# Performance work log

Measured on AMD Instinct MI355X. Metric: run time of the kernel, lower is better.

## Reference

```python
import jax, jax.numpy as jnp
import numpy as np

NUM_EXPERTS = 64
Z_LOSS_COEF = 0.001
AUX_LOSS_COEF = 0.001
GROUPS, TOKENS = 64, 8192


def setup_inputs() -> dict:
    key = jax.random.key(0)
    k1, = jax.random.split(key, 1)
    router_logits = jax.random.normal(k1, (GROUPS, TOKENS, NUM_EXPERTS), dtype=jnp.float32)
    attention_mask = jnp.ones((GROUPS, TOKENS), dtype=jnp.int32)  # unused by forward, kept for fidelity
    return {"router_logits": router_logits, "attention_mask": attention_mask, "expert_capacity": 160}


def reference(router_logits, attention_mask, expert_capacity):
    g, t, e = router_logits.shape

    # --- router z-loss: mean over (groups, tokens) of logsumexp^2 ---
    log_z = jax.nn.logsumexp(router_logits, axis=-1)            # [g, t]
    z_loss = jnp.sum(log_z * log_z) / (g * t)

    # --- softmax probs ---
    router_probs = jax.nn.softmax(router_logits, axis=-1)       # [g, t, e]

    # --- recompute expert indices with capacity masking ---
    expert_index = jnp.argmax(router_probs, axis=-1)            # [g, t]
    oh = jax.nn.one_hot(expert_index, e, dtype=jnp.int32)       # [g, t, e]
    token_priority = jnp.cumsum(oh, axis=-2)                    # running count per expert
    capacity_mask = token_priority <= expert_capacity
    oh_masked = oh * capacity_mask.astype(jnp.int32)
    # if token dropped (row all zero), argmax -> 0, matching torch semantics
    expert_index = jnp.argmax(oh_masked, axis=-1)               # [g, t]

    # --- load-balancing aux loss ---
    expert_mask = jax.nn.one_hot(expert_index, e, dtype=jnp.float32)  # [g, t, e]
    tokens_per_group_and_expert = jnp.mean(expert_mask, axis=-2)       # [g, e]
    router_prob_per_group_and_expert = jnp.mean(router_probs, axis=-2) # [g, e]
    aux_loss = jnp.mean(tokens_per_group_and_expert * router_prob_per_group_and_expert) * (e ** 2)

    return Z_LOSS_COEF * z_loss + AUX_LOSS_COEF * aux_loss
```

## Files before the change

### kernel.cpp

```cpp
#include <hip/hip_runtime.h>

#define NG 64
#define NT 8192
#define NE 64
#define Z_COEF 0.001f
#define A_COEF 0.001f

#define BLK 512
#define ITERS 4
#define TPW 64
#define TPB 512
#define NBLK (NG * (NT / TPB))

#define LOG2E 1.44269504088896340736f
#define LN2   0.69314718055994530942f
#define BIGIDX 1048576

#define DPP_XOR1  0xB1
#define DPP_XOR2  0x4E
#define DPP_HMIRR 0x141
#define DPP_MIRR  0x140

template <int CTRL>
__device__ __forceinline__ float fdpp(float x) {
    return __int_as_float(__builtin_amdgcn_mov_dpp(__float_as_int(x), CTRL, 0xF, 0xF, true));
}
template <int CTRL>
__device__ __forceinline__ int idpp(int x) {
    return __builtin_amdgcn_mov_dpp(x, CTRL, 0xF, 0xF, true);
}


__global__ __launch_bounds__(BLK) void router_main(
    const float* __restrict__ logits,
    float* __restrict__ pps,
    unsigned int* __restrict__ pcnt,
    float* __restrict__ pz)
{
    const int tid  = threadIdx.x;
    const int lane = tid & 63;
    const int wv   = tid >> 6;
    const int c    = lane & 15;
    const int cb   = c << 2;

    const int g     = blockIdx.x >> 4;
    const int tbase = (blockIdx.x & 15) * TPB + wv * TPW;

    const float* p0 = logits + ((size_t)g * NT + tbase) * NE + lane * 4;

    __shared__ float        s_ps[NE];
    __shared__ unsigned int s_cnt[NE];
    __shared__ float        s_z;
    if (tid < NE) { s_ps[tid] = 0.f; s_cnt[tid] = 0u; }
    if (tid == 0) s_z = 0.f;
    __syncthreads();

    float accp[4] = {0.f, 0.f, 0.f, 0.f};
    float accz = 0.f;

    for (int it = 0; it < ITERS; ++it) {
        const float* pi = p0 + (size_t)it * 1024;
        float4 cur[4];
#pragma unroll
        for (int k = 0; k < 4; ++k)
            cur[k] = *reinterpret_cast<const float4*>(pi + k * 256);

#pragma unroll
        for (int k = 0; k < 4; ++k) {
            const float v0 = cur[k].x, v1 = cur[k].y, v2 = cur[k].z, v3 = cur[k].w;

            float m = fmaxf(fmaxf(v0, v1), fmaxf(v2, v3));
            m = fmaxf(m, fdpp<DPP_XOR1>(m));
            m = fmaxf(m, fdpp<DPP_XOR2>(m));
            m = fmaxf(m, fdpp<DPP_HMIRR>(m));
            m = fmaxf(m, fdpp<DPP_MIRR>(m));

            const float e0 = exp2f((v0 - m) * LOG2E);
            const float e1 = exp2f((v1 - m) * LOG2E);
            const float e2 = exp2f((v2 - m) * LOG2E);
            const float e3 = exp2f((v3 - m) * LOG2E);
            float s = (e0 + e1) + (e2 + e3);

            int me = BIGIDX;
            if (v3 == m) me = cb + 3;
            if (v2 == m) me = cb + 2;
            if (v1 == m) me = cb + 1;
            if (v0 == m) me = cb + 0;
            me = min(me, idpp<DPP_XOR1>(me));
            me = min(me, idpp<DPP_XOR2>(me));
            me = min(me, idpp<DPP_HMIRR>(me));
            me = min(me, idpp<DPP_MIRR>(me));

            s += fdpp<DPP_XOR1>(s);
            s += fdpp<DPP_XOR2>(s);
            s += fdpp<DPP_HMIRR>(s);
            s += fdpp<DPP_MIRR>(s);

            const float inv = __builtin_amdgcn_rcpf(s);
            accp[0] = fmaf(e0, inv, accp[0]);
            accp[1] = fmaf(e1, inv, accp[1]);
            accp[2] = fmaf(e2, inv, accp[2]);
            accp[3] = fmaf(e3, inv, accp[3]);

            const float lz = fmaf(__log2f(s), LN2, m);
            accz = fmaf(lz, lz, accz);

            if (c == 0)
                atomicAdd(&s_cnt[me], 1u);
        }
    }

#pragma unroll
    for (int j = 0; j < 4; ++j) {
        accp[j] += __shfl_xor(accp[j], 16);
        accp[j] += __shfl_xor(accp[j], 32);
    }
    if (lane < 16) {
#pragma unroll
        for (int j = 0; j < 4; ++j) atomicAdd(&s_ps[(c << 2) + j], accp[j]);
    }
    accz += __shfl_xor(accz, 1);
    accz += __shfl_xor(accz, 2);
    accz += __shfl_xor(accz, 4);
    accz += __shfl_xor(accz, 8);
    accz += __shfl_xor(accz, 16);
    accz += __shfl_xor(accz, 32);
    if (lane == 0) atomicAdd(&s_z, accz * 0.0625f);
    __syncthreads();

    const int row = blockIdx.x;
    if (tid < NE) {
        pps [row * NE + tid] = s_ps[tid];
        pcnt[row * NE + tid] = s_cnt[tid];
    }
    if (tid == 0) pz[row] = s_z;
}

__global__ __launch_bounds__(1024) void router_final(
    const float* __restrict__ pps,
    const unsigned int* __restrict__ pcnt,
    const float* __restrict__ pz,
    const int* __restrict__ capp,
    float* __restrict__ out)
{
    const int tid  = threadIdx.x;
    const int lane = tid & 63;
    const int w    = tid >> 6;
    const unsigned int C = (unsigned int)(*capp);

    __shared__ float s_aux[16];
    __shared__ float s_zz[16];

    float acc = 0.f;
#pragma unroll
    for (int gi = 0; gi < NG / 16; ++gi) {
        const int g = w + gi * 16;
        unsigned int n = 0u;
        float        P = 0.f;
#pragma unroll
        for (int b = 0; b < 16; ++b) {
            const int row = g * 16 + b;
            n += pcnt[row * NE + lane];
            P += pps [row * NE + lane];
        }
        float ovf = (n > C) ? (float)(n - C) : 0.f;
#pragma unroll
        for (int off = 1; off <= 32; off <<= 1) ovf += __shfl_xor(ovf, off);
        float ce = fminf((float)n, (float)C);
        if (lane == 0) ce += ovf;
        acc += ce * P;
    }
#pragma unroll
    for (int off = 1; off <= 32; off <<= 1) acc += __shfl_xor(acc, off);
    if (lane == 0) s_aux[w] = acc;

    float zz = pz[tid];
#pragma unroll
    for (int off = 1; off <= 32; off <<= 1) zz += __shfl_xor(zz, off);
    if (lane == 0) s_zz[w] = zz;
    __syncthreads();

    if (tid == 0) {
        float A = 0.f, Z = 0.f;
#pragma unroll
        for (int i = 0; i < 16; ++i) { A += s_aux[i]; Z += s_zz[i]; }
        const float aux_loss = A * ((float)NE / ((float)NG * (float)NT * (float)NT));
        const float z_loss   = Z / ((float)NG * (float)NT);
        out[0] = Z_COEF * z_loss + A_COEF * aux_loss;
    }
}

extern "C" void kernel_launch(void* const* d_in, const int* in_sizes, int n_in,
                              void* d_out, int out_size, void* d_ws, size_t ws_size,
                              hipStream_t stream)
{
    const float* logits = (const float*)d_in[0];
    const int* cap = (const int*)d_in[2];

    float*        pps  = (float*)d_ws;
    unsigned int* pcnt = (unsigned int*)((char*)d_ws + (size_t)NBLK * NE * 4);
    float*        pz   = (float*)((char*)d_ws + 2ull * NBLK * NE * 4);

    router_main<<<NBLK, BLK, 0, stream>>>(logits, pps, pcnt, pz);
    router_final<<<1, 1024, 0, stream>>>(pps, pcnt, pz, cap, (float*)d_out);
}
```

Baseline: 36.97 us.

## Parallelize final reduction across groups with atomic last-block completion

The single 1024-thread final-reduction block becomes 64 one-wave blocks, one per group. Each block atomically adds its aux and z partials to a global accumulator, and the last block to finish, found through a done counter, writes the output. The first block of the main kernel zeroes the accumulators and counter. This spreads the final reduction's memory reads across many CUs, at the cost of global atomics and a counter that must be reset on every call, and it makes the float summation order nondeterministic.

```diff
diff --git a/kernel.cpp b/kernel.cpp
--- a/kernel.cpp
+++ b/kernel.cpp
@@ -35,13 +35,21 @@
     const float* __restrict__ logits,
     float* __restrict__ pps,
     unsigned int* __restrict__ pcnt,
-    float* __restrict__ pz)
+    float* __restrict__ pz,
+    float* __restrict__ accbuf,
+    unsigned int* __restrict__ donep)
 {
     const int tid  = threadIdx.x;
     const int lane = tid & 63;
     const int wv   = tid >> 6;
     const int c    = lane & 15;
     const int cb   = c << 2;
+
+    if (blockIdx.x == 0 && tid == 0) {
+        accbuf[0] = 0.f;
+        accbuf[1] = 0.f;
+        *donep    = 0u;
+    }
 
     const int g     = blockIdx.x >> 4;
     const int tbase = (blockIdx.x & 15) * TPB + wv * TPW;
@@ -117,7 +125,7 @@
     }
     if (lane < 16) {
 #pragma unroll
-        for (int j = 0; j < 4; ++j) atomicAdd(&s_ps[(c << 2) + j], accp[j]);
+        for (int j = 0; j < 4; ++j) atomicAdd(&s_ps[cb + j], accp[j]);
     }
     accz += __shfl_xor(accz, 1);
     accz += __shfl_xor(accz, 2);
@@ -136,54 +144,57 @@
     if (tid == 0) pz[row] = s_z;
 }
 
-__global__ __launch_bounds__(1024) void router_final(
+__global__ __launch_bounds__(64) void router_final(
     const float* __restrict__ pps,
     const unsigned int* __restrict__ pcnt,
     const float* __restrict__ pz,
     const int* __restrict__ capp,
+    float* __restrict__ accbuf,
+    unsigned int* __restrict__ donep,
     float* __restrict__ out)
 {
-    const int tid  = threadIdx.x;
-    const int lane = tid & 63;
-    const int w    = tid >> 6;
+    const int lane = threadIdx.x;
+    const int g    = blockIdx.x;
     const unsigned int C = (unsigned int)(*capp);
 
-    __shared__ float s_aux[16];
-    __shared__ float s_zz[16];
-
-    float acc = 0.f;
-#pragma unroll
-    for (int gi = 0; gi < NG / 16; ++gi) {
-        const int g = w + gi * 16;
-        unsigned int n = 0u;
-        float        P = 0.f;
-#pragma unroll
-        for (int b = 0; b < 16; ++b) {
-            const int row = g * 16 + b;
-            n += pcnt[row * NE + lane];
-            P += pps [row * NE + lane];
-        }
-        float ovf = (n > C) ? (float)(n - C) : 0.f;
-#pragma unroll
-        for (int off = 1; off <= 32; off <<= 1) ovf += __shfl_xor(ovf, off);
-        float ce = fminf((float)n, (float)C);
-        if (lane == 0) ce += ovf;
-        acc += ce * P;
-    }
-#pragma unroll
-    for (int off = 1; off <= 32; off <<= 1) acc += __shfl_xor(acc, off);
-    if (lane == 0) s_aux[w] = acc;
-
-    float zz = pz[tid];
-#pragma unroll
-    for (int off = 1; off <= 32; off <<= 1) zz += __shfl_xor(zz, off);
-    if (lane == 0) s_zz[w] = zz;
-    __syncthreads();
-
-    if (tid == 0) {
-        float A = 0.f, Z = 0.f;
-#pragma unroll
-        for (int i = 0; i < 16; ++i) { A += s_aux[i]; Z += s_zz[i]; }
+    unsigned int n = 0u;
+    float        P = 0.f;
+#pragma unroll
+    for (int b = 0; b < 16; ++b) {
+        const int row = g * 16 + b;
+        n += pcnt[row * NE + lane];
+        P += pps [row * NE + lane];
+    }
+
+    float ovf = (n > C) ? (float)(n - C) : 0.f;
+#pragma unroll
+    for (int off = 1; off <= 32; off <<= 1) ovf += __shfl_xor(ovf, off);
+
+    float ce = fminf((float)n, (float)C);
+    if (lane == 0) ce += ovf;
+    float term = ce * P;
+#pragma unroll
+    for (int off = 1; off <= 32; off <<= 1) term += __shfl_xor(term, off);
+
+    float zz = (lane < 16) ? pz[g * 16 + lane] : 0.f;
+#pragma unroll
+    for (int off = 1; off <= 8; off <<= 1) zz += __shfl_xor(zz, off);
+
+    if (lane == 0) {
+        atomicAdd(&accbuf[0], term);
+        atomicAdd(&accbuf[1], zz);
+    }
+    __threadfence();
+
+    bool last = false;
+    if (lane == 0)
+        last = (atomicAdd(donep, 1u) == (unsigned int)(NG - 1));
+
+    if (last) {
+        const float A = __hip_atomic_load(&accbuf[0], __ATOMIC_RELAXED,
+                                          __HIP_MEMORY_SCOPE_AGENT);
+        const float Z = __hip_atomic_load(&accbuf[1], __ATOMIC_RELAXED,
+                                          __HIP_MEMORY_SCOPE_AGENT);
         const float aux_loss = A * ((float)NE / ((float)NG * (float)NT * (float)NT));
         const float z_loss   = Z / ((float)NG * (float)NT);
         out[0] = Z_COEF * z_loss + A_COEF * aux_loss;
@@ -197,10 +208,13 @@
     const float* logits = (const float*)d_in[0];
     const int* cap = (const int*)d_in[2];
 
-    float*        pps  = (float*)d_ws;
-    unsigned int* pcnt = (unsigned int*)((char*)d_ws + (size_t)NBLK * NE * 4);
-    float*        pz   = (float*)((char*)d_ws + 2ull * NBLK * NE * 4);
-
-    router_main<<<NBLK, BLK, 0, stream>>>(logits, pps, pcnt, pz);
-    router_final<<<1, 1024, 0, stream>>>(pps, pcnt, pz, cap, (float*)d_out);
-}
+    float*        pps    = (float*)d_ws;
+    unsigned int* pcnt   = (unsigned int*)((char*)d_ws + (size_t)NBLK * NE * 4);
+    float*        pz     = (float*)((char*)d_ws + 2ull * NBLK * NE * 4);
+    float*        accbuf = (float*)((char*)d_ws + 2ull * NBLK * NE * 4 + NBLK * 4);
+    unsigned int* donep  = (unsigned int*)((char*)d_ws + 2ull * NBLK * NE * 4 + NBLK * 4 + 8);
+
+    router_main<<<NBLK, BLK, 0, stream>>>(logits, pps, pcnt, pz, accbuf, donep);
+    router_final<<<NG, 64, 0, stream>>>(pps, pcnt, pz, cap, accbuf, donep,
+                                        (float*)d_out);
+}
```

After: 35.18 us. -4.8%, faster.
